# Kernel optimization log

Measured on AMD Instinct MI355X. Metric: run time of the kernel, lower is better.

Reference implementation:

```python
import jax, jax.numpy as jnp
import numpy as np


def setup_inputs() -> dict:
    key = jax.random.key(0)
    k1, k2, k3, k4, k5 = jax.random.split(key, 5)
    bs, ns, seq_len = 32, 512, 1024
    n_heads, d_r, d_model = 8, 64, 256
    return {
        "x": jax.random.normal(k1, (bs, ns, seq_len), dtype=jnp.float32),
        "routers": jax.random.normal(k2, (n_heads, d_r, d_model), dtype=jnp.float32),
        "w_kv_weight": jax.random.normal(k3, (n_heads * d_model, seq_len), dtype=jnp.float32) * 0.02,
        "proj_weight": jax.random.normal(k4, (seq_len, n_heads * d_model), dtype=jnp.float32) * 0.02,
        "proj_bias": jax.random.normal(k5, (seq_len,), dtype=jnp.float32) * 0.02,
    }


def reference(x, routers, w_kv_weight, proj_weight, proj_bias):
    # x: (bs, ns, seq_len); routers: (H, d_r, d_model)
    bs, ns, _ = x.shape
    H, d_r, d_model = routers.shape
    qk_scale = 1.0 / jnp.sqrt(jnp.asarray(d_model, x.dtype))
    # shared K=V projection: (bs, ns, H*d_model) -> (bs, H, ns, d_model)
    kv = (x @ w_kv_weight.T).reshape(bs, ns, H, d_model).transpose(0, 2, 1, 3)
    # low-rank learned queries attend over the ns axis: (bs, H, d_r, ns)
    attn_score = jnp.einsum('hrd,bhnd->bhrn', routers, kv) * qk_scale
    attn_weight = jax.nn.softmax(attn_score, axis=-1)
    # dropout is identity in eval/reference mode
    out = jnp.einsum('bhrn,bhnd->bhrd', attn_weight, kv)  # (bs, H, d_r, d_model)
    out = out.transpose(0, 2, 1, 3).reshape(bs, d_r, H * d_model)
    out = out @ proj_weight.T + proj_bias  # (bs, d_r, seq_len)
    return out, attn_weight
```

## Files before the change

### kernel.cpp

```cpp
#include <hip/hip_runtime.h>
#include <hip/hip_bf16.h>


typedef __attribute__((ext_vector_type(8))) short short8;
typedef __attribute__((ext_vector_type(4))) short short4v;
typedef __attribute__((ext_vector_type(4))) float f32x4;
typedef __attribute__((ext_vector_type(4))) unsigned int uint4v;
typedef __attribute__((ext_vector_type(4))) unsigned short ushort4v;

__device__ inline unsigned short f2bf(float f) {
  unsigned int u = __float_as_uint(f);
  u += 0x7FFFu + ((u >> 16) & 1u);
  return (unsigned short)(u >> 16);
}

__device__ __forceinline__ void async_copy16(unsigned short* lds, const unsigned short* g) {
  __builtin_amdgcn_global_load_lds(
      (const __attribute__((address_space(1))) unsigned int*)g,
      (__attribute__((address_space(3))) unsigned int*)lds,
      16, 0, 0);
}

__global__ __launch_bounds__(256) void cast_f32_bf16(const float* __restrict__ in,
                                                     unsigned short* __restrict__ out, int n4) {
  int i = blockIdx.x * 256 + threadIdx.x;
  if (i >= n4) return;
  float4 v = ((const float4*)in)[i];
  ushort4v w; w.x = f2bf(v.x); w.y = f2bf(v.y); w.z = f2bf(v.z); w.w = f2bf(v.w);
  ((ushort4v*)out)[i] = w;
}

__global__ __launch_bounds__(512, 1) void gemm1_8phase(
    const unsigned short* __restrict__ A, const unsigned short* __restrict__ B,
    unsigned short* __restrict__ C, int lda, int ldb, int ldc, int K, int nWGn)
{
  __shared__ __align__(16) unsigned short sA[2][2][8192];
  __shared__ __align__(16) unsigned short sB[2][2][8192];

  const int tid = threadIdx.x;
  const int cpx = gridDim.x >> 3;
  const int swz = (blockIdx.x & 7) * cpx + (blockIdx.x >> 3);
  const int bn = swz % nWGn, bm = swz / nWGn;

  const int wave = tid >> 6, lane = tid & 63;
  const int wm = wave >> 2, wn = wave & 3;
  const int lr = lane & 15, ls = lane >> 4;
  const int lsw8 = (ls ^ ((lr >> 1) & 3)) * 8;

  const int r0 = tid >> 2;
  const int sl0 = (tid & 3) ^ ((tid >> 3) & 3);
  const unsigned short* gA = A + (long long)(bm * 256 + r0) * lda + sl0 * 8;
  const unsigned short* gB = B + (long long)(bn * 256 + r0) * ldb + sl0 * 8;
  const long long lda128 = (long long)128 * lda, ldb128 = (long long)128 * ldb;

#define STA(b_, k_, t_) { const unsigned short* g_ = gA + (t_) * 64 + (k_) * 32; \
    async_copy16(&sA[b_][k_][tid * 8], g_); \
    async_copy16(&sA[b_][k_][4096 + tid * 8], g_ + lda128); }
#define STB(b_, k_, t_) { const unsigned short* g_ = gB + (t_) * 64 + (k_) * 32; \
    async_copy16(&sB[b_][k_][tid * 8], g_); \
    async_copy16(&sB[b_][k_][4096 + tid * 8], g_ + ldb128); }

  f32x4 acc[8][4];
  #pragma unroll
  for (int mi = 0; mi < 8; ++mi)
    #pragma unroll
    for (int ni = 0; ni < 4; ++ni)
      acc[mi][ni] = f32x4{0.f, 0.f, 0.f, 0.f};

  const int KT = K >> 6;
  STB(0, 0, 0) STA(0, 0, 0) STB(0, 1, 0) STA(0, 1, 0)
  if (KT > 1) {
    STB(1, 0, 1) STA(1, 0, 1) STB(1, 1, 1)
    asm volatile("s_waitcnt vmcnt(6)" ::: "memory");
  } else {
    asm volatile("s_waitcnt vmcnt(0)" ::: "memory");
  }
  __builtin_amdgcn_s_barrier();
  __builtin_amdgcn_sched_barrier(0);

  for (int t = 0; t < KT; ++t) {
    const int b = t & 1, nb = b ^ 1;
    const bool hasT1 = (t + 1) < KT, hasT2 = (t + 2) < KT;
    short8 af[4], bf[4];

    #pragma unroll
    for (int mi = 0; mi < 4; ++mi)
      af[mi] = *(const short8*)&sA[b][0][(wm * 128 + mi * 16 + lr) * 32 + lsw8];
    #pragma unroll
    for (int ni = 0; ni < 4; ++ni)
      bf[ni] = *(const short8*)&sB[b][0][(wn * 64 + ni * 16 + lr) * 32 + lsw8];
    if (hasT1) { STA(nb, 1, t + 1) }
    __builtin_amdgcn_s_setprio(1);
    #pragma unroll
    for (int mi = 0; mi < 4; ++mi)
      #pragma unroll
      for (int ni = 0; ni < 4; ++ni)
        acc[mi][ni] = __builtin_amdgcn_mfma_f32_16x16x32_bf16(af[mi], bf[ni], acc[mi][ni], 0, 0, 0);
    __builtin_amdgcn_s_setprio(0);
    __builtin_amdgcn_s_barrier();

    #pragma unroll
    for (int mi = 0; mi < 4; ++mi)
      af[mi] = *(const short8*)&sA[b][0][(wm * 128 + (4 + mi) * 16 + lr) * 32 + lsw8];
    if (hasT2) { STB(b, 0, t + 2) }
    __builtin_amdgcn_s_setprio(1);
    #pragma unroll
    for (int mi = 0; mi < 4; ++mi)
      #pragma unroll
      for (int ni = 0; ni < 4; ++ni)
        acc[4 + mi][ni] = __builtin_amdgcn_mfma_f32_16x16x32_bf16(af[mi], bf[ni], acc[4 + mi][ni], 0, 0, 0);
    __builtin_amdgcn_s_setprio(0);
    __builtin_amdgcn_s_barrier();

    #pragma unroll
    for (int mi = 0; mi < 4; ++mi)
      af[mi] = *(const short8*)&sA[b][1][(wm * 128 + mi * 16 + lr) * 32 + lsw8];
    #pragma unroll
    for (int ni = 0; ni < 4; ++ni)
      bf[ni] = *(const short8*)&sB[b][1][(wn * 64 + ni * 16 + lr) * 32 + lsw8];
    if (hasT2) { STA(b, 0, t + 2) }
    __builtin_amdgcn_s_setprio(1);
    #pragma unroll
    for (int mi = 0; mi < 4; ++mi)
      #pragma unroll
      for (int ni = 0; ni < 4; ++ni)
        acc[mi][ni] = __builtin_amdgcn_mfma_f32_16x16x32_bf16(af[mi], bf[ni], acc[mi][ni], 0, 0, 0);
    __builtin_amdgcn_s_setprio(0);
    __builtin_amdgcn_s_barrier();

    #pragma unroll
    for (int mi = 0; mi < 4; ++mi)
      af[mi] = *(const short8*)&sA[b][1][(wm * 128 + (4 + mi) * 16 + lr) * 32 + lsw8];
    if (hasT2) { STB(b, 1, t + 2) }
    __builtin_amdgcn_s_setprio(1);
    #pragma unroll
    for (int mi = 0; mi < 4; ++mi)
      #pragma unroll
      for (int ni = 0; ni < 4; ++ni)
        acc[4 + mi][ni] = __builtin_amdgcn_mfma_f32_16x16x32_bf16(af[mi], bf[ni], acc[4 + mi][ni], 0, 0, 0);
    __builtin_amdgcn_s_setprio(0);
    if (t == KT - 2) {
      asm volatile("s_waitcnt vmcnt(0)" ::: "memory");
    } else if (t < KT - 2) {
      asm volatile("s_waitcnt vmcnt(6)" ::: "memory");
    }
    __builtin_amdgcn_s_barrier();
    __builtin_amdgcn_sched_barrier(0);
  }
#undef STA
#undef STB

  #pragma unroll
  for (int mi = 0; mi < 8; ++mi) {
    #pragma unroll
    for (int ni = 0; ni < 4; ++ni) {
      int row = bm * 256 + wm * 128 + mi * 16 + ls * 4;
      int col = bn * 256 + wn * 64 + ni * 16 + lr;
      #pragma unroll
      for (int r = 0; r < 4; ++r)
        C[(long long)(row + r) * ldc + col] = f2bf(acc[mi][ni][r]);
    }
  }
}

template<int BM,int BN,int BK,int WM,int WN,bool TRANS_B,bool A_F32,bool OUT_BF16,bool DO_SCALE,bool DO_BIAS>
__global__ __launch_bounds__(256) void gemm_bt(
    const void* __restrict__ Av, const unsigned short* __restrict__ Bp,
    void* __restrict__ Cv, const float* __restrict__ bias,
    int lda, int ldb, int ldc, int K, int nWGn,
    long long strAo, long long strAi, long long strBo, long long strBi,
    long long strCo, long long strCi, int binner, float scale)
{
  constexpr int PADA = 8;
  constexpr int PADB = TRANS_B ? 4 : 8;
  constexpr int STRA = BK + PADA;
  constexpr int STRB = BK + PADB;
  constexpr int NWN = BN / WN;
  constexpr int MF = WM / 16, NF = WN / 16;
  __shared__ __align__(16) unsigned short lds_a[BM * STRA];
  __shared__ __align__(16) unsigned short lds_b[BN * STRB];

  const int tid = threadIdx.x;
  const int bn = blockIdx.x % nWGn;
  const int bm = blockIdx.x / nWGn;
  const int batch = blockIdx.y;
  const int bo = batch / binner, bi = batch % binner;

  const int wave = tid >> 6, lane = tid & 63;
  const int wm = wave / NWN, wn = wave % NWN;
  const int lr = lane & 15;
  const int lk = (lane >> 4) * 8;

  const long long abase = bo*strAo + bi*strAi + (long long)bm*BM*lda;
  const long long bbase = bo*strBo + bi*strBi;

  f32x4 acc[MF][NF];
  #pragma unroll
  for (int mi = 0; mi < MF; ++mi)
    #pragma unroll
    for (int ni = 0; ni < NF; ++ni)
      acc[mi][ni] = f32x4{0.f, 0.f, 0.f, 0.f};

  for (int k0 = 0; k0 < K; k0 += BK) {
    if constexpr (A_F32) {
      const float* Af = (const float*)Av + abase + k0;
      #pragma unroll
      for (int i = 0; i < BM*BK/1024; ++i) {
        int c = i*256 + tid;
        int r = c / (BK/4);
        int kc = (c % (BK/4)) * 4;
        float4 v = *(const float4*)(Af + (long long)r*lda + kc);
        ushort4v w; w.x=f2bf(v.x); w.y=f2bf(v.y); w.z=f2bf(v.z); w.w=f2bf(v.w);
        *(ushort4v*)&lds_a[r*STRA + kc] = w;
      }
    } else {
      const unsigned short* Ab2 = (const unsigned short*)Av + abase + k0;
      #pragma unroll
      for (int i = 0; i < BM*BK/2048; ++i) {
        int c = i*256 + tid;
        int r = c / (BK/8);
        int kc = (c % (BK/8)) * 8;
        *(uint4v*)&lds_a[r*STRA + kc] = *(const uint4v*)(Ab2 + (long long)r*lda + kc);
      }
    }
    if constexpr (!TRANS_B) {
      const unsigned short* Bb2 = Bp + bbase + (long long)bn*BN*ldb + k0;
      #pragma unroll
      for (int i = 0; i < BN*BK/2048; ++i) {
        int c = i*256 + tid;
        int r = c / (BK/8);
        int kc = (c % (BK/8)) * 8;
        *(uint4v*)&lds_b[r*STRB + kc] = *(const uint4v*)(Bb2 + (long long)r*ldb + kc);
      }
    } else {
      const unsigned short* Bb2 = Bp + bbase + (long long)k0*ldb + (long long)bn*BN;
      #pragma unroll
      for (int i = 0; i < BN*BK/2048; ++i) {
        int c = i*256 + tid;
        int kr = c / (BN/8);
        int nc = (c % (BN/8)) * 8;
        uint4v v = *(const uint4v*)(Bb2 + (long long)kr*ldb + nc);
        const unsigned short* pv = (const unsigned short*)&v;
        #pragma unroll
        for (int j = 0; j < 8; ++j) lds_b[(nc+j)*STRB + kr] = pv[j];
      }
    }
    __syncthreads();

    #pragma unroll
    for (int kk = 0; kk < BK/32; ++kk) {
      short8 af[MF]; short8 bfr[NF];
      #pragma unroll
      for (int mi = 0; mi < MF; ++mi)
        af[mi] = *(const short8*)&lds_a[(wm*WM + mi*16 + lr)*STRA + kk*32 + lk];
      #pragma unroll
      for (int ni = 0; ni < NF; ++ni) {
        if constexpr (TRANS_B) {
          int base = (wn*WN + ni*16 + lr)*STRB + kk*32 + lk;
          short4v lo = *(const short4v*)&lds_b[base];
          short4v hi = *(const short4v*)&lds_b[base + 4];
          short8 t; t[0]=lo[0]; t[1]=lo[1]; t[2]=lo[2]; t[3]=lo[3];
                    t[4]=hi[0]; t[5]=hi[1]; t[6]=hi[2]; t[7]=hi[3];
          bfr[ni] = t;
        } else {
          bfr[ni] = *(const short8*)&lds_b[(wn*WN + ni*16 + lr)*STRB + kk*32 + lk];
        }
      }
      #pragma unroll
      for (int mi = 0; mi < MF; ++mi)
        #pragma unroll
        for (int ni = 0; ni < NF; ++ni)
          acc[mi][ni] = __builtin_amdgcn_mfma_f32_16x16x32_bf16(af[mi], bfr[ni], acc[mi][ni], 0, 0, 0);
    }
    __syncthreads();
  }

  const long long cbase = bo*strCo + bi*strCi;
  const int cr0 = (lane >> 4) * 4;
  #pragma unroll
  for (int mi = 0; mi < MF; ++mi) {
    #pragma unroll
    for (int ni = 0; ni < NF; ++ni) {
      int row = bm*BM + wm*WM + mi*16 + cr0;
      int col = bn*BN + wn*WN + ni*16 + lr;
      float badd = DO_BIAS ? bias[col] : 0.f;
      #pragma unroll
      for (int r = 0; r < 4; ++r) {
        float x = acc[mi][ni][r];
        if constexpr (DO_SCALE) x *= scale;
        x += badd;
        long long addr = cbase + (long long)(row + r)*ldc + col;
        if constexpr (OUT_BF16) ((unsigned short*)Cv)[addr] = f2bf(x);
        else                    ((float*)Cv)[addr] = x;
      }
    }
  }
}

__global__ __launch_bounds__(256) void softmax_rows(float* __restrict__ sc,
                                                    unsigned short* __restrict__ P) {
  int row = blockIdx.x * 4 + (threadIdx.x >> 6);
  int lane = threadIdx.x & 63;
  float* rp = sc + (long long)row * 512 + lane * 8;
  float4 a = *(const float4*)rp;
  float4 b = *(const float4*)(rp + 4);
  float v[8] = {a.x, a.y, a.z, a.w, b.x, b.y, b.z, b.w};
  float m = v[0];
  #pragma unroll
  for (int i = 1; i < 8; ++i) m = fmaxf(m, v[i]);
  #pragma unroll
  for (int d = 1; d < 64; d <<= 1) m = fmaxf(m, __shfl_xor(m, d, 64));
  float s = 0.f;
  #pragma unroll
  for (int i = 0; i < 8; ++i) { v[i] = __expf(v[i] - m); s += v[i]; }
  #pragma unroll
  for (int d = 1; d < 64; d <<= 1) s += __shfl_xor(s, d, 64);
  float inv = 1.0f / s;
  #pragma unroll
  for (int i = 0; i < 8; ++i) v[i] *= inv;
  float4 oa = {v[0], v[1], v[2], v[3]}, ob = {v[4], v[5], v[6], v[7]};
  *(float4*)rp = oa; *(float4*)(rp + 4) = ob;
  unsigned short* pp = P + (long long)row * 512 + lane * 8;
  ushort4v w0, w1;
  w0.x=f2bf(v[0]); w0.y=f2bf(v[1]); w0.z=f2bf(v[2]); w0.w=f2bf(v[3]);
  w1.x=f2bf(v[4]); w1.y=f2bf(v[5]); w1.z=f2bf(v[6]); w1.w=f2bf(v[7]);
  *(ushort4v*)pp = w0; *(ushort4v*)(pp + 4) = w1;
}

extern "C" void kernel_launch(void* const* d_in, const int* in_sizes, int n_in,
                              void* d_out, int out_size, void* d_ws, size_t ws_size,
                              hipStream_t stream) {
  const float* x       = (const float*)d_in[0];
  const float* routers = (const float*)d_in[1];
  const float* wkv     = (const float*)d_in[2];
  const float* projw   = (const float*)d_in[3];
  const float* pbias   = (const float*)d_in[4];

  char* ws = (char*)d_ws;
  unsigned short* wkv_b   = (unsigned short*)(ws);
  unsigned short* projw_b = (unsigned short*)(ws +  4194304);
  unsigned short* kv_b    = (unsigned short*)(ws +  8388608);
  unsigned short* xb        = (unsigned short*)(ws + 75497472);
  unsigned short* routers_b = (unsigned short*)(ws + 75497472);
  unsigned short* P_b       = (unsigned short*)(ws + 75759616);
  unsigned short* ao_b      = (unsigned short*)(ws + 92536832);

  float* out0  = (float*)d_out;
  float* attnw = out0 + 2097152;

  cast_f32_bf16<<<2048,  256, 0, stream>>>(wkv,   wkv_b,   524288);
  cast_f32_bf16<<<2048,  256, 0, stream>>>(projw, projw_b, 524288);
  cast_f32_bf16<<<16384, 256, 0, stream>>>(x,     xb,      4194304);

  gemm1_8phase<<<512, 512, 0, stream>>>(xb, wkv_b, kv_b, 1024, 1024, 2048, 1024, 8);

  cast_f32_bf16<<<128, 256, 0, stream>>>(routers, routers_b, 32768);

  gemm_bt<64,128,64,64,32,false,false,false,true,false><<<dim3(4,256), 256, 0, stream>>>(
      routers_b, kv_b, attnw, nullptr, 256, 2048, 512, 256, 4,
      0, 16384, 1048576, 256, 262144, 32768, 8, 0.0625f);

  softmax_rows<<<4096, 256, 0, stream>>>(attnw, P_b);

  gemm_bt<64,128,64,64,32,true,false,true,false,false><<<dim3(2,256), 256, 0, stream>>>(
      P_b, kv_b, ao_b, nullptr, 512, 2048, 2048, 512, 2,
      262144, 32768, 1048576, 256, 131072, 256, 8, 1.0f);

  gemm_bt<64,128,64,64,32,false,false,false,false,true><<<dim3(256,1), 256, 0, stream>>>(
      ao_b, projw_b, out0, pbias, 2048, 2048, 1024, 2048, 8,
      0,0, 0,0, 0,0, 1, 1.0f);
}
```

Measured before the change: 184.2 us.

## Double-buffer MFMA operand fragments in registers across GEMM sub-steps

Restructures the bf16 256x256 GEMM main loop so LDS fragment reads for the next MFMA sub-block are issued before the current 16-MFMA block runs. It ping-pongs between two register sets (aX/aY, bX/bY) and uses explicit lgkmcnt waits and sched_barrier fences to control ordering. The next tile's first fragments are prefetched at the end of each iteration, after the vmcnt wait. This hides LDS read latency behind matrix-core work, at the cost of more VGPRs. It also reads the next buffer before the cross-wave barrier that follows the async-copy wait, which could race with other waves' in-flight copies.

```diff
diff --git a/kernel.cpp b/kernel.cpp
--- a/kernel.cpp
+++ b/kernel.cpp
@@ -59,6 +59,17 @@
 #define STB(b_, k_, t_) { const unsigned short* g_ = gB + (t_) * 64 + (k_) * 32; \
     async_copy16(&sB[b_][k_][tid * 8], g_); \
     async_copy16(&sB[b_][k_][4096 + tid * 8], g_ + ldb128); }
+#define LDA4(dst, b_, k_, mh_) { _Pragma("unroll") \
+    for (int mi = 0; mi < 4; ++mi) \
+      dst[mi] = *(const short8*)&sA[b_][k_][(wm * 128 + ((mh_) * 4 + mi) * 16 + lr) * 32 + lsw8]; }
+#define LDB4(dst, b_, k_) { _Pragma("unroll") \
+    for (int ni = 0; ni < 4; ++ni) \
+      dst[ni] = *(const short8*)&sB[b_][k_][(wn * 64 + ni * 16 + lr) * 32 + lsw8]; }
+#define MFMA16(ah, src_a, src_b) { _Pragma("unroll") \
+    for (int mi = 0; mi < 4; ++mi) { _Pragma("unroll") \
+      for (int ni = 0; ni < 4; ++ni) \
+        acc[(ah) * 4 + mi][ni] = __builtin_amdgcn_mfma_f32_16x16x32_bf16(src_a[mi], src_b[ni], acc[(ah) * 4 + mi][ni], 0, 0, 0); } }
+#define FENCE() __builtin_amdgcn_sched_barrier(0)
 
   f32x4 acc[8][4];
   #pragma unroll
@@ -76,79 +87,73 @@
     asm volatile("s_waitcnt vmcnt(0)" ::: "memory");
   }
   __builtin_amdgcn_s_barrier();
-  __builtin_amdgcn_sched_barrier(0);
+  FENCE();
+
+  short8 aX[4], aY[4], bX[4], bY[4];
+  LDA4(aX, 0, 0, 0)
+  LDB4(bX, 0, 0)
 
   for (int t = 0; t < KT; ++t) {
     const int b = t & 1, nb = b ^ 1;
     const bool hasT1 = (t + 1) < KT, hasT2 = (t + 2) < KT;
-    short8 af[4], bf[4];
-
-    #pragma unroll
-    for (int mi = 0; mi < 4; ++mi)
-      af[mi] = *(const short8*)&sA[b][0][(wm * 128 + mi * 16 + lr) * 32 + lsw8];
-    #pragma unroll
-    for (int ni = 0; ni < 4; ++ni)
-      bf[ni] = *(const short8*)&sB[b][0][(wn * 64 + ni * 16 + lr) * 32 + lsw8];
+
     if (hasT1) { STA(nb, 1, t + 1) }
+    LDA4(aY, b, 0, 1)
+    asm volatile("s_waitcnt lgkmcnt(4)" ::: "memory");
+    FENCE();
     __builtin_amdgcn_s_setprio(1);
-    #pragma unroll
-    for (int mi = 0; mi < 4; ++mi)
-      #pragma unroll
-      for (int ni = 0; ni < 4; ++ni)
-        acc[mi][ni] = __builtin_amdgcn_mfma_f32_16x16x32_bf16(af[mi], bf[ni], acc[mi][ni], 0, 0, 0);
+    MFMA16(0, aX, bX)
     __builtin_amdgcn_s_setprio(0);
     __builtin_amdgcn_s_barrier();
-
-    #pragma unroll
-    for (int mi = 0; mi < 4; ++mi)
-      af[mi] = *(const short8*)&sA[b][0][(wm * 128 + (4 + mi) * 16 + lr) * 32 + lsw8];
+    FENCE();
+
     if (hasT2) { STB(b, 0, t + 2) }
+    LDA4(aX, b, 1, 0)
+    LDB4(bY, b, 1)
+    asm volatile("s_waitcnt lgkmcnt(8)" ::: "memory");
+    FENCE();
     __builtin_amdgcn_s_setprio(1);
-    #pragma unroll
-    for (int mi = 0; mi < 4; ++mi)
-      #pragma unroll
-      for (int ni = 0; ni < 4; ++ni)
-        acc[4 + mi][ni] = __builtin_amdgcn_mfma_f32_16x16x32_bf16(af[mi], bf[ni], acc[4 + mi][ni], 0, 0, 0);
+    MFMA16(1, aY, bX)
     __builtin_amdgcn_s_setprio(0);
     __builtin_amdgcn_s_barrier();
-
-    #pragma unroll
-    for (int mi = 0; mi < 4; ++mi)
-      af[mi] = *(const short8*)&sA[b][1][(wm * 128 + mi * 16 + lr) * 32 + lsw8];
-    #pragma unroll
-    for (int ni = 0; ni < 4; ++ni)
-      bf[ni] = *(const short8*)&sB[b][1][(wn * 64 + ni * 16 + lr) * 32 + lsw8];
+    FENCE();
+
     if (hasT2) { STA(b, 0, t + 2) }
+    LDA4(aY, b, 1, 1)
+    asm volatile("s_waitcnt lgkmcnt(4)" ::: "memory");
+    FENCE();
     __builtin_amdgcn_s_setprio(1);
-    #pragma unroll
-    for (int mi = 0; mi < 4; ++mi)
-      #pragma unroll
-      for (int ni = 0; ni < 4; ++ni)
-        acc[mi][ni] = __builtin_amdgcn_mfma_f32_16x16x32_bf16(af[mi], bf[ni], acc[mi][ni], 0, 0, 0);
+    MFMA16(0, aX, bY)
     __builtin_amdgcn_s_setprio(0);
     __builtin_amdgcn_s_barrier();
-
-    #pragma unroll
-    for (int mi = 0; mi < 4; ++mi)
-      af[mi] = *(const short8*)&sA[b][1][(wm * 128 + (4 + mi) * 16 + lr) * 32 + lsw8];
+    FENCE();
+
     if (hasT2) { STB(b, 1, t + 2) }
+    if (hasT1) {
+      if (t == KT - 2) {
+        asm volatile("s_waitcnt vmcnt(0)" ::: "memory");
+      } else {
+        asm volatile("s_waitcnt vmcnt(6)" ::: "memory");
+      }
+      LDA4(aX, nb, 0, 0)
+      LDB4(bX, nb, 0)
+      asm volatile("s_waitcnt lgkmcnt(8)" ::: "memory");
+    } else {
+      asm volatile("s_waitcnt lgkmcnt(0)" ::: "memory");
+    }
+    FENCE();
     __builtin_amdgcn_s_setprio(1);
-    #pragma unroll
-    for (int mi = 0; mi < 4; ++mi)
-      #pragma unroll
-      for (int ni = 0; ni < 4; ++ni)
-        acc[4 + mi][ni] = __builtin_amdgcn_mfma_f32_16x16x32_bf16(af[mi], bf[ni], acc[4 + mi][ni], 0, 0, 0);
+    MFMA16(1, aY, bY)
     __builtin_amdgcn_s_setprio(0);
-    if (t == KT - 2) {
-      asm volatile("s_waitcnt vmcnt(0)" ::: "memory");
-    } else if (t < KT - 2) {
-      asm volatile("s_waitcnt vmcnt(6)" ::: "memory");
-    }
     __builtin_amdgcn_s_barrier();
-    __builtin_amdgcn_sched_barrier(0);
+    FENCE();
   }
 #undef STA
 #undef STB
+#undef LDA4
+#undef LDB4
+#undef MFMA16
+#undef FENCE
 
   #pragma unroll
   for (int mi = 0; mi < 8; ++mi) {
```

After: 190.2 us. 1.03x slower.

## Fuse score GEMM with softmax and merge input casts into one kernel

Applied to the files above, without the earlier changes.

Replaces the router cast, score GEMM and separate softmax kernel with one kernel per (batch, head). It computes the 64x512 score tile with MFMA, reduces row max and sum across waves in LDS, and writes both the fp32 attention weights and the bf16 P directly. This removes the round trip of writing fp32 scores and reading them back, and also merges the three fp32-to-bf16 cast launches into one. The cost is only 256 blocks of 1024 threads with a simple non-pipelined load loop, so occupancy and latency hiding may be worse than before.

```diff
diff --git a/kernel.cpp b/kernel.cpp
--- a/kernel.cpp
+++ b/kernel.cpp
@@ -21,13 +21,18 @@
       16, 0, 0);
 }
 
-__global__ __launch_bounds__(256) void cast_f32_bf16(const float* __restrict__ in,
-                                                     unsigned short* __restrict__ out, int n4) {
+__global__ __launch_bounds__(256) void cast_all(
+    const float* __restrict__ x, const float* __restrict__ wkv, const float* __restrict__ projw,
+    unsigned short* __restrict__ xb, unsigned short* __restrict__ wkv_b,
+    unsigned short* __restrict__ projw_b) {
   int i = blockIdx.x * 256 + threadIdx.x;
-  if (i >= n4) return;
-  float4 v = ((const float4*)in)[i];
+  const float* src; unsigned short* dst; int off;
+  if (i < 524288)        { src = wkv;   dst = wkv_b;   off = i; }
+  else if (i < 1048576)  { src = projw; dst = projw_b; off = i - 524288; }
+  else                   { src = x;     dst = xb;      off = i - 1048576; }
+  float4 v = ((const float4*)src)[off];
   ushort4v w; w.x = f2bf(v.x); w.y = f2bf(v.y); w.z = f2bf(v.z); w.w = f2bf(v.w);
-  ((ushort4v*)out)[i] = w;
+  ((ushort4v*)dst)[off] = w;
 }
 
 __global__ __launch_bounds__(512, 1) void gemm1_8phase(
@@ -159,6 +164,95 @@
       #pragma unroll
       for (int r = 0; r < 4; ++r)
         C[(long long)(row + r) * ldc + col] = f2bf(acc[mi][ni][r]);
+    }
+  }
+}
+
+__global__ __launch_bounds__(1024, 1) void score_softmax(
+    const float* __restrict__ routers,
+    const unsigned short* __restrict__ kv,
+    float* __restrict__ attnw,
+    unsigned short* __restrict__ P)
+{
+  __shared__ __align__(16) unsigned short lds_a[64 * 72];
+  __shared__ __align__(16) unsigned short lds_b[512 * 72];
+  __shared__ float redmax[64][4];
+  __shared__ float redsum[64][4];
+
+  const int bh = blockIdx.x;
+  const int b = bh >> 3, h = bh & 7;
+  const int tid = threadIdx.x;
+  const int wave = tid >> 6, lane = tid & 63;
+  const int wm = wave >> 2, wn = wave & 3;
+  const int lr = lane & 15, ls = lane >> 4;
+  const int lk = ls * 8;
+
+  const unsigned short* kvb = kv + (long long)b * 512 * 2048 + h * 256;
+  const float* Rh = routers + h * 16384;
+
+  f32x4 acc[8];
+  #pragma unroll
+  for (int ni = 0; ni < 8; ++ni) acc[ni] = f32x4{0.f, 0.f, 0.f, 0.f};
+
+  for (int k0 = 0; k0 < 256; k0 += 64) {
+    {
+      int r = tid >> 4, kc = (tid & 15) * 4;
+      float4 v = *(const float4*)(Rh + r * 256 + k0 + kc);
+      ushort4v w; w.x = f2bf(v.x); w.y = f2bf(v.y); w.z = f2bf(v.z); w.w = f2bf(v.w);
+      *(ushort4v*)&lds_a[r * 72 + kc] = w;
+    }
+    #pragma unroll
+    for (int i = 0; i < 4; ++i) {
+      int c = i * 1024 + tid;
+      int r = c >> 3, kc = (c & 7) * 8;
+      *(uint4v*)&lds_b[r * 72 + kc] = *(const uint4v*)(kvb + (long long)r * 2048 + k0 + kc);
+    }
+    __syncthreads();
+    #pragma unroll
+    for (int kk = 0; kk < 2; ++kk) {
+      short8 af = *(const short8*)&lds_a[(wm * 16 + lr) * 72 + kk * 32 + lk];
+      #pragma unroll
+      for (int ni = 0; ni < 8; ++ni) {
+        short8 bf = *(const short8*)&lds_b[(wn * 128 + ni * 16 + lr) * 72 + kk * 32 + lk];
+        acc[ni] = __builtin_amdgcn_mfma_f32_16x16x32_bf16(af, bf, acc[ni], 0, 0, 0);
+      }
+    }
+    __syncthreads();
+  }
+
+  #pragma unroll
+  for (int q = 0; q < 4; ++q) {
+    int row = wm * 16 + ls * 4 + q;
+    float m = -1e30f;
+    #pragma unroll
+    for (int ni = 0; ni < 8; ++ni) { acc[ni][q] *= 0.0625f; m = fmaxf(m, acc[ni][q]); }
+    #pragma unroll
+    for (int d = 1; d < 16; d <<= 1) m = fmaxf(m, __shfl_xor(m, d, 64));
+    if (lr == 0) redmax[row][wn] = m;
+  }
+  __syncthreads();
+  #pragma unroll
+  for (int q = 0; q < 4; ++q) {
+    int row = wm * 16 + ls * 4 + q;
+    float M = fmaxf(fmaxf(redmax[row][0], redmax[row][1]), fmaxf(redmax[row][2], redmax[row][3]));
+    float s = 0.f;
+    #pragma unroll
+    for (int ni = 0; ni < 8; ++ni) { float p = __expf(acc[ni][q] - M); acc[ni][q] = p; s += p; }
+    #pragma unroll
+    for (int d = 1; d < 16; d <<= 1) s += __shfl_xor(s, d, 64);
+    if (lr == 0) redsum[row][wn] = s;
+  }
+  __syncthreads();
+  #pragma unroll
+  for (int q = 0; q < 4; ++q) {
+    int row = wm * 16 + ls * 4 + q;
+    float inv = 1.0f / (redsum[row][0] + redsum[row][1] + redsum[row][2] + redsum[row][3]);
+    long long base = (long long)bh * 32768 + row * 512 + wn * 128;
+    #pragma unroll
+    for (int ni = 0; ni < 8; ++ni) {
+      float wv = acc[ni][q] * inv;
+      attnw[base + ni * 16 + lr] = wv;
+      P[base + ni * 16 + lr] = f2bf(wv);
     }
   }
 }
@@ -297,36 +391,6 @@
   }
 }
 
-__global__ __launch_bounds__(256) void softmax_rows(float* __restrict__ sc,
-                                                    unsigned short* __restrict__ P) {
-  int row = blockIdx.x * 4 + (threadIdx.x >> 6);
-  int lane = threadIdx.x & 63;
-  float* rp = sc + (long long)row * 512 + lane * 8;
-  float4 a = *(const float4*)rp;
-  float4 b = *(const float4*)(rp + 4);
-  float v[8] = {a.x, a.y, a.z, a.w, b.x, b.y, b.z, b.w};
-  float m = v[0];
-  #pragma unroll
-  for (int i = 1; i < 8; ++i) m = fmaxf(m, v[i]);
-  #pragma unroll
-  for (int d = 1; d < 64; d <<= 1) m = fmaxf(m, __shfl_xor(m, d, 64));
-  float s = 0.f;
-  #pragma unroll
-  for (int i = 0; i < 8; ++i) { v[i] = __expf(v[i] - m); s += v[i]; }
-  #pragma unroll
-  for (int d = 1; d < 64; d <<= 1) s += __shfl_xor(s, d, 64);
-  float inv = 1.0f / s;
-  #pragma unroll
-  for (int i = 0; i < 8; ++i) v[i] *= inv;
-  float4 oa = {v[0], v[1], v[2], v[3]}, ob = {v[4], v[5], v[6], v[7]};
-  *(float4*)rp = oa; *(float4*)(rp + 4) = ob;
-  unsigned short* pp = P + (long long)row * 512 + lane * 8;
-  ushort4v w0, w1;
-  w0.x=f2bf(v[0]); w0.y=f2bf(v[1]); w0.z=f2bf(v[2]); w0.w=f2bf(v[3]);
-  w1.x=f2bf(v[4]); w1.y=f2bf(v[5]); w1.z=f2bf(v[6]); w1.w=f2bf(v[7]);
-  *(ushort4v*)pp = w0; *(ushort4v*)(pp + 4) = w1;
-}
-
 extern "C" void kernel_launch(void* const* d_in, const int* in_sizes, int n_in,
                               void* d_out, int out_size, void* d_ws, size_t ws_size,
                               hipStream_t stream) {
@@ -340,27 +404,18 @@
   unsigned short* wkv_b   = (unsigned short*)(ws);
   unsigned short* projw_b = (unsigned short*)(ws +  4194304);
   unsigned short* kv_b    = (unsigned short*)(ws +  8388608);
-  unsigned short* xb        = (unsigned short*)(ws + 75497472);
-  unsigned short* routers_b = (unsigned short*)(ws + 75497472);
-  unsigned short* P_b       = (unsigned short*)(ws + 75759616);
-  unsigned short* ao_b      = (unsigned short*)(ws + 92536832);
+  unsigned short* xb      = (unsigned short*)(ws + 75497472);
+  unsigned short* P_b     = (unsigned short*)(ws + 75759616);
+  unsigned short* ao_b    = (unsigned short*)(ws + 92536832);
 
   float* out0  = (float*)d_out;
   float* attnw = out0 + 2097152;
 
-  cast_f32_bf16<<<2048,  256, 0, stream>>>(wkv,   wkv_b,   524288);
-  cast_f32_bf16<<<2048,  256, 0, stream>>>(projw, projw_b, 524288);
-  cast_f32_bf16<<<16384, 256, 0, stream>>>(x,     xb,      4194304);
+  cast_all<<<20480, 256, 0, stream>>>(x, wkv, projw, xb, wkv_b, projw_b);
 
   gemm1_8phase<<<512, 512, 0, stream>>>(xb, wkv_b, kv_b, 1024, 1024, 2048, 1024, 8);
 
-  cast_f32_bf16<<<128, 256, 0, stream>>>(routers, routers_b, 32768);
-
-  gemm_bt<64,128,64,64,32,false,false,false,true,false><<<dim3(4,256), 256, 0, stream>>>(
-      routers_b, kv_b, attnw, nullptr, 256, 2048, 512, 256, 4,
-      0, 16384, 1048576, 256, 262144, 32768, 8, 0.0625f);
-
-  softmax_rows<<<4096, 256, 0, stream>>>(attnw, P_b);
+  score_softmax<<<256, 1024, 0, stream>>>(routers, kv_b, attnw, P_b);
 
   gemm_bt<64,128,64,64,32,true,false,true,false,false><<<dim3(2,256), 256, 0, stream>>>(
       P_b, kv_b, ao_b, nullptr, 512, 2048, 2048, 512, 2,
```

New measurement: 171.0 us. 1.08x faster.
